# Performance work log

Measured on AMD Instinct MI355X. Metric: run time of the kernel, lower is better.

Reference implementation:

```python
import jax, jax.numpy as jnp
import numpy as np

B, T, S0 = 8, 4, 4096
D_MODEL, H, D, R, RANK = 2048, 16, 128, 64, 512
C = D - R  # content dim = 64


def _rope(x, positions):
    # x: [B, H, T, R]; rotate-half style RoPE as in the torch module
    half = x.shape[-1] // 2
    inv_freq = 1.0 / (10000.0 ** (jnp.arange(half, dtype=jnp.float32) / half))
    freqs = positions.astype(jnp.float32)[:, None] * inv_freq[None, :]  # [T, half]
    cos = jnp.cos(freqs)[None, None].astype(x.dtype)
    sin = jnp.sin(freqs)[None, None].astype(x.dtype)
    x1, x2 = x[..., :half], x[..., half:]
    return jnp.concatenate([x1 * cos - x2 * sin, x1 * sin + x2 * cos], axis=-1)


def setup_inputs() -> dict:
    key = jax.random.key(0)
    ks = jax.random.split(key, 9)
    s = 0.02
    return {
        "x": jax.random.normal(ks[0], (B, T, D_MODEL), jnp.float32),
        "cache_c_kv": jax.random.normal(ks[1], (B, S0, RANK), jnp.float32),
        "cache_k_rope": jax.random.normal(ks[2], (B, S0, H, R), jnp.float32),
        "w_q": jax.random.normal(ks[3], (D_MODEL, H * C), jnp.float32) * s,
        "w_q_rope": jax.random.normal(ks[4], (D_MODEL, H * R), jnp.float32) * s,
        "w_kv_down": jax.random.normal(ks[5], (D_MODEL, RANK), jnp.float32) * s,
        "w_kv_up": jax.random.normal(ks[6], (RANK, H * D), jnp.float32) * s,
        "w_k_rope": jax.random.normal(ks[7], (D_MODEL, H * R), jnp.float32) * s,
        "w_out": jax.random.normal(ks[8], (H * D, D_MODEL), jnp.float32) * s,
    }


def reference(x, cache_c_kv, cache_k_rope, w_q, w_q_rope, w_kv_down, w_kv_up, w_k_rope, w_out):
    cache_len = cache_c_kv.shape[1]
    positions = jnp.arange(cache_len, cache_len + T)

    # queries
    q_content = (x @ w_q).reshape(B, T, H, C).transpose(0, 2, 1, 3)        # [B,H,T,C]
    q_rope = (x @ w_q_rope).reshape(B, T, H, R).transpose(0, 2, 1, 3)      # [B,H,T,R]
    q_rope = _rope(q_rope, positions)
    q = jnp.concatenate([q_content, q_rope], axis=-1)                       # [B,H,T,D]

    # new compressed kv + rope keys, append to cache
    c_kv_new = x @ w_kv_down                                                # [B,T,RANK]
    k_rope_new = (x @ w_k_rope).reshape(B, T, H, R).transpose(0, 2, 1, 3)
    k_rope_new = _rope(k_rope_new, positions).transpose(0, 2, 1, 3)         # [B,T,H,R]
    c_kv = jnp.concatenate([cache_c_kv, c_kv_new], axis=1)                  # [B,S,RANK]
    k_rope = jnp.concatenate([cache_k_rope, k_rope_new], axis=1)            # [B,S,H,R]

    # decompress full cache every step (the expensive MLA pattern)
    S = c_kv.shape[1]
    kv = (c_kv @ w_kv_up).reshape(B, S, H, D)                               # [B,S,H,D]
    k_content = kv[..., :C].transpose(0, 2, 1, 3)                           # [B,H,S,C]
    v = kv.transpose(0, 2, 1, 3)                                            # [B,H,S,D]
    k = jnp.concatenate([k_content, k_rope.transpose(0, 2, 1, 3)], axis=-1) # [B,H,S,D]

    # kv_cache present => is_prefill False => no causal mask (faithful to source)
    scale = 1.0 / jnp.sqrt(jnp.asarray(D, dtype=q.dtype))
    scores = jnp.einsum('bhtd,bhsd->bhts', q, k) * scale
    attn = jax.nn.softmax(scores, axis=-1)
    out = jnp.einsum('bhts,bhsd->bhtd', attn, v)                            # [B,H,T,D]
    out = out.transpose(0, 2, 1, 3).reshape(B, T, H * D)
    return out @ w_out                                                       # [B,T,D_MODEL]
```

## Files before the change

### kernel.cpp

```cpp
#include <hip/hip_runtime.h>
#include <cmath>

#define BB 8
#define TT 4
#define HH 16
#define DDIM 128
#define RRDIM 64
#define CCDIM 64
#define RANKC 512
#define DMODEL 2048
#define S0C 4096
#define NQ 64
#define HD 2048
#define NACT 3584
#define NSC 65
#define SPAD 4160
#define SCALE_ATT 0.08838834764831845f

#define AIDX(row, kk) ((row)*132 + (((row)>>2)<<2) + (kk))

static __device__ __forceinline__ unsigned short f2bf(float x) {
  unsigned u = __float_as_uint(x);
  u += 0x7FFFu + ((u >> 16) & 1u);
  return (unsigned short)(u >> 16);
}
static __device__ __forceinline__ float bf2f(unsigned v16) {
  return __uint_as_float(v16 << 16);
}
static __device__ __forceinline__ unsigned pk2(float a, float b) {
  return (unsigned)f2bf(a) | ((unsigned)f2bf(b) << 16);
}

__global__ __launch_bounds__(256) void k_proj4(const float* __restrict__ A,
                                               const float* __restrict__ w0,
                                               const float* __restrict__ w1,
                                               const float* __restrict__ w2,
                                               const float* __restrict__ w3,
                                               float* __restrict__ part) {
  __shared__ float a_lds[4352];
  const int tid = threadIdx.x;
  const int cb = blockIdx.x;
  const int k0 = blockIdx.y * 128;
  const float* W; int N, lc0, off;
  if (cb < 8)       { W = w0; N = 1024; lc0 = cb * 128;        off = 0; }
  else if (cb < 16) { W = w1; N = 1024; lc0 = (cb - 8) * 128;  off = 1024; }
  else if (cb < 20) { W = w2; N = 512;  lc0 = (cb - 16) * 128; off = 2048; }
  else              { W = w3; N = 1024; lc0 = (cb - 20) * 128; off = 2560; }
  {
    const int row = tid >> 3;
    const int kseg = (tid & 7) * 16;
    const float4* s4 = reinterpret_cast<const float4*>(A + (size_t)row * DMODEL + k0 + kseg);
    float4 v0 = s4[0], v1 = s4[1], v2 = s4[2], v3 = s4[3];
    *reinterpret_cast<float4*>(&a_lds[AIDX(row, kseg)])      = v0;
    *reinterpret_cast<float4*>(&a_lds[AIDX(row, kseg + 4)])  = v1;
    *reinterpret_cast<float4*>(&a_lds[AIDX(row, kseg + 8)])  = v2;
    *reinterpret_cast<float4*>(&a_lds[AIDX(row, kseg + 12)]) = v3;
  }
  __syncthreads();
  const int cg = tid & 31;
  const int rg = tid >> 5;
  float acc[4][4];
  #pragma unroll
  for (int r = 0; r < 4; ++r)
    #pragma unroll
    for (int c = 0; c < 4; ++c) acc[r][c] = 0.f;
  #pragma unroll 4
  for (int kk = 0; kk < 128; ++kk) {
    const float4 w4 = *reinterpret_cast<const float4*>(W + (size_t)(k0 + kk) * N + lc0 + cg * 4);
    const float wv[4] = {w4.x, w4.y, w4.z, w4.w};
    #pragma unroll
    for (int r = 0; r < 4; ++r) {
      const float av = a_lds[AIDX(rg * 4 + r, kk)];
      #pragma unroll
      for (int c = 0; c < 4; ++c) acc[r][c] = fmaf(av, wv[c], acc[r][c]);
    }
  }
  #pragma unroll
  for (int r = 0; r < 4; ++r) {
    float4 o = make_float4(acc[r][0], acc[r][1], acc[r][2], acc[r][3]);
    *reinterpret_cast<float4*>(part + ((size_t)blockIdx.y * 32 + rg * 4 + r) * NACT + off + lc0 + cg * 4) = o;
  }
}

__global__ __launch_bounds__(256) void k_proj(const float* __restrict__ A,
                                              const float* __restrict__ W,
                                              float* __restrict__ part,
                                              int N, int NTOT, int coloff) {
  __shared__ float a_lds[4352];
  const int tid = threadIdx.x;
  const int c0 = blockIdx.x * 128;
  const int k0 = blockIdx.y * 128;
  {
    const int row = tid >> 3;
    const int kseg = (tid & 7) * 16;
    const float4* s4 = reinterpret_cast<const float4*>(A + (size_t)row * DMODEL + k0 + kseg);
    float4 v0 = s4[0], v1 = s4[1], v2 = s4[2], v3 = s4[3];
    *reinterpret_cast<float4*>(&a_lds[AIDX(row, kseg)])      = v0;
    *reinterpret_cast<float4*>(&a_lds[AIDX(row, kseg + 4)])  = v1;
    *reinterpret_cast<float4*>(&a_lds[AIDX(row, kseg + 8)])  = v2;
    *reinterpret_cast<float4*>(&a_lds[AIDX(row, kseg + 12)]) = v3;
  }
  __syncthreads();
  const int cg = tid & 31;
  const int rg = tid >> 5;
  float acc[4][4];
  #pragma unroll
  for (int r = 0; r < 4; ++r)
    #pragma unroll
    for (int c = 0; c < 4; ++c) acc[r][c] = 0.f;
  #pragma unroll 4
  for (int kk = 0; kk < 128; ++kk) {
    const float4 w4 = *reinterpret_cast<const float4*>(W + (size_t)(k0 + kk) * N + c0 + cg * 4);
    const float wv[4] = {w4.x, w4.y, w4.z, w4.w};
    #pragma unroll
    for (int r = 0; r < 4; ++r) {
      const float av = a_lds[AIDX(rg * 4 + r, kk)];
      #pragma unroll
      for (int c = 0; c < 4; ++c) acc[r][c] = fmaf(av, wv[c], acc[r][c]);
    }
  }
  #pragma unroll
  for (int r = 0; r < 4; ++r) {
    float4 o = make_float4(acc[r][0], acc[r][1], acc[r][2], acc[r][3]);
    *reinterpret_cast<float4*>(part + ((size_t)blockIdx.y * 32 + rg * 4 + r) * NTOT + coloff + c0 + cg * 4) = o;
  }
}

__global__ __launch_bounds__(256) void k_reduce(const float* __restrict__ part,
                                                float* __restrict__ out, int total, int nsplit) {
  int g = blockIdx.x * 256 + threadIdx.x;
  if (g >= total) return;
  float s = 0.f;
  #pragma unroll 4
  for (int c = 0; c < nsplit; ++c) s += part[(size_t)c * total + g];
  out[g] = s;
}

__global__ __launch_bounds__(256) void k_qlatrope(const float* __restrict__ act,
                                                  const float* __restrict__ wup,
                                                  float* __restrict__ qlat,
                                                  float* __restrict__ qrope,
                                                  float* __restrict__ ckvn,
                                                  float* __restrict__ krn) {
  __shared__ float wt[64 * 132];
  __shared__ float a_s[32 * 68];
  const int tid = threadIdx.x;
  const int bx = blockIdx.x;
  if (bx < 64) {
    const int h = bx & 15;
    const int r0 = (bx >> 4) * 128;
    {
      const int r = tid >> 1;
      const int cseg = (tid & 1) * 32;
      const float* src = wup + (size_t)(r0 + r) * HD + h * DDIM + cseg;
      #pragma unroll
      for (int u = 0; u < 8; ++u) {
        const float4 v = *reinterpret_cast<const float4*>(src + u * 4);
        wt[(cseg + u * 4 + 0) * 132 + r] = v.x;
        wt[(cseg + u * 4 + 1) * 132 + r] = v.y;
        wt[(cseg + u * 4 + 2) * 132 + r] = v.z;
        wt[(cseg + u * 4 + 3) * 132 + r] = v.w;
      }
    }
    {
      const int bt = tid >> 3;
      const int cseg = (tid & 7) * 8;
      const float4* s4 = reinterpret_cast<const float4*>(act + (size_t)bt * NACT + h * CCDIM + cseg);
      float4 v0 = s4[0], v1 = s4[1];
      *reinterpret_cast<float4*>(&a_s[bt * 68 + cseg])     = v0;
      *reinterpret_cast<float4*>(&a_s[bt * 68 + cseg + 4]) = v1;
    }
    __syncthreads();
    const int r = tid & 127;
    const int bth = tid >> 7;
    float acc[16];
    #pragma unroll
    for (int i = 0; i < 16; ++i) acc[i] = 0.f;
    #pragma unroll 8
    for (int c = 0; c < 64; ++c) {
      const float wv = wt[c * 132 + r];
      #pragma unroll
      for (int i = 0; i < 16; ++i)
        acc[i] = fmaf(a_s[(bth * 16 + i) * 68 + c], wv, acc[i]);
    }
    #pragma unroll
    for (int i = 0; i < 16; ++i) {
      const int bt = bth * 16 + i;
      const int b = bt >> 2, t = bt & 3;
      qlat[((size_t)(b * NQ) + h * TT + t) * RANKC + r0 + r] = acc[i];
    }
    return;
  }
  int g = (bx - 64) * 256 + tid;
  if (g < BB * TT * HH * 32) {
    const int hj = g & 31;
    const int h = (g >> 5) & 15;
    const int t = (g >> 9) & 3;
    const int b = g >> 11;
    const float* arow = act + (size_t)(b * TT + t) * NACT + 1024 + h * RRDIM;
    const float x1 = arow[hj], x2 = arow[hj + 32];
    const double fr = (double)(S0C + t) * pow(10000.0, -(double)hj / 32.0);
    const float cs = (float)cos(fr), sn = (float)sin(fr);
    const int qi = h * TT + t;
    qrope[((size_t)b * NQ + qi) * RRDIM + hj]      = x1 * cs - x2 * sn;
    qrope[((size_t)b * NQ + qi) * RRDIM + hj + 32] = x1 * sn + x2 * cs;
    return;
  }
  g -= BB * TT * HH * 32;
  if (g < BB * TT * HH * 32) {
    const int hj = g & 31;
    const int h = (g >> 5) & 15;
    const int t = (g >> 9) & 3;
    const int b = g >> 11;
    const float* arow = act + (size_t)(b * TT + t) * NACT + 2560 + h * RRDIM;
    const float x1 = arow[hj], x2 = arow[hj + 32];
    const double fr = (double)(S0C + t) * pow(10000.0, -(double)hj / 32.0);
    const float cs = (float)cos(fr), sn = (float)sin(fr);
    krn[((size_t)(b * TT + t) * HH + h) * RRDIM + hj]      = x1 * cs - x2 * sn;
    krn[((size_t)(b * TT + t) * HH + h) * RRDIM + hj + 32] = x1 * sn + x2 * cs;
    return;
  }
  g -= BB * TT * HH * 32;
  if (g < BB * TT * RANKC) {
    ckvn[g] = act[(size_t)(g >> 9) * NACT + 2048 + (g & 511)];
  }
}

__global__ __launch_bounds__(256) void k_rscore(const float* __restrict__ cache_kr,
                                                const float* __restrict__ krn,
                                                const float* __restrict__ qrope,
                                                float* __restrict__ rs) {
  const int bh = blockIdx.x;
  const int b = bh >> 4, h = bh & 15;
  const int tid = threadIdx.x;
  const int ql = tid & 3;
  float4 qf[4][4];
  const float* qrb = qrope + ((size_t)b * NQ + h * TT) * RRDIM;
  #pragma unroll
  for (int t = 0; t < 4; ++t)
    #pragma unroll
    for (int u = 0; u < 4; ++u)
      qf[t][u] = *reinterpret_cast<const float4*>(qrb + t * RRDIM + ql * 16 + u * 4);
  const int s0 = blockIdx.y * 512;
  #pragma unroll 1
  for (int pass = 0; pass < 8; ++pass) {
    const int s = s0 + pass * 64 + (tid >> 2);
    if (s < 4100) {
      const float* krow = (s < S0C)
        ? cache_kr + (((size_t)b * S0C + s) * HH + h) * RRDIM
        : krn + (((size_t)b * TT + (s - S0C)) * HH + h) * RRDIM;
      float p[4] = {0.f, 0.f, 0.f, 0.f};
      #pragma unroll
      for (int u = 0; u < 4; ++u) {
        const float4 kv = *reinterpret_cast<const float4*>(krow + ql * 16 + u * 4);
        #pragma unroll
        for (int t = 0; t < 4; ++t) {
          p[t] += kv.x * qf[t][u].x + kv.y * qf[t][u].y
                + kv.z * qf[t][u].z + kv.w * qf[t][u].w;
        }
      }
      #pragma unroll
      for (int t = 0; t < 4; ++t) {
        p[t] += __shfl_xor(p[t], 1, 4);
        p[t] += __shfl_xor(p[t], 2, 4);
      }
      rs[((size_t)bh * 4 + ql) * SPAD + s] = p[ql];
    }
  }
}

__global__ __launch_bounds__(256) void k_attn(
    const float* __restrict__ cache_ckv, const float* __restrict__ ckvn,
    const float* __restrict__ rs, const float* __restrict__ qlat,
    float* __restrict__ ml, unsigned short* __restrict__ olat) {
  __shared__ float sm[13056];
  float* const A0 = sm;
  float* const A1 = sm + 2176;
  float* const B0 = sm + 4352;
  float* const B1 = sm + 6528;
  float* const p_t = sm + 8704;
  float* const CS0 = sm;
  float* const CS1 = sm + 4352;

  const int tid = threadIdx.x;
  const int ty = tid >> 4, tx = tid & 15;
  const int b = blockIdx.x, chunk = blockIdx.y;
  const int scnt = (chunk < 64) ? 64 : TT;
  const float* ckv = (chunk < 64)
      ? cache_ckv + ((size_t)b * S0C + (size_t)chunk * 64) * RANKC
      : ckvn + (size_t)b * TT * RANKC;
  const float* qlb = qlat + (size_t)b * NQ * RANKC;

  float acc[4][4];
  {
    const int sg = chunk * 64 + tx * 4;
    #pragma unroll
    for (int i = 0; i < 4; ++i) {
      const float4 v = *reinterpret_cast<const float4*>(
          rs + (((size_t)(b * HH + ty)) * 4 + i) * SPAD + sg);
      acc[i][0] = v.x; acc[i][1] = v.y; acc[i][2] = v.z; acc[i][3] = v.w;
    }
  }

  const int row = tid >> 2;
  const int kb = (tid & 3) * 8;
  float4 ra0, ra1, rb0, rb1;
  auto loadAB = [&](int kc) {
    const float4* a4 = reinterpret_cast<const float4*>(qlb + (size_t)row * RANKC + kc + kb);
    ra0 = a4[0]; ra1 = a4[1];
    if (row < scnt) {
      const float4* b4 = reinterpret_cast<const float4*>(ckv + (size_t)row * RANKC + kc + kb);
      rb0 = b4[0]; rb1 = b4[1];
    } else { rb0 = make_float4(0.f, 0.f, 0.f, 0.f); rb1 = rb0; }
  };
  auto writeAB = [&](float* aD, float* bD) {
    aD[(kb+0)*68+row]=ra0.x; aD[(kb+1)*68+row]=ra0.y; aD[(kb+2)*68+row]=ra0.z; aD[(kb+3)*68+row]=ra0.w;
    aD[(kb+4)*68+row]=ra1.x; aD[(kb+5)*68+row]=ra1.y; aD[(kb+6)*68+row]=ra1.z; aD[(kb+7)*68+row]=ra1.w;
    bD[(kb+0)*68+row]=rb0.x; bD[(kb+1)*68+row]=rb0.y; bD[(kb+2)*68+row]=rb0.z; bD[(kb+3)*68+row]=rb0.w;
    bD[(kb+4)*68+row]=rb1.x; bD[(kb+5)*68+row]=rb1.y; bD[(kb+6)*68+row]=rb1.z; bD[(kb+7)*68+row]=rb1.w;
  };
  loadAB(0);
  writeAB(A0, B0);
  __syncthreads();
  for (int kt = 0; kt < 16; ++kt) {
    if (kt < 15) loadAB((kt + 1) * 32);
    const float* aC = (kt & 1) ? A1 : A0;
    const float* bC = (kt & 1) ? B1 : B0;
    #pragma unroll 8
    for (int kk = 0; kk < 32; ++kk) {
      const float4 av = *reinterpret_cast<const float4*>(&aC[kk * 68 + ty * 4]);
      const float4 bv = *reinterpret_cast<const float4*>(&bC[kk * 68 + tx * 4]);
      const float a_[4] = {av.x, av.y, av.z, av.w};
      const float b_[4] = {bv.x, bv.y, bv.z, bv.w};
      #pragma unroll
      for (int i = 0; i < 4; ++i)
        #pragma unroll
        for (int j = 0; j < 4; ++j)
          acc[i][j] = fmaf(a_[i], b_[j], acc[i][j]);
    }
    if (kt < 15) writeAB((kt & 1) ? A0 : A1, (kt & 1) ? B0 : B1);
    __syncthreads();
  }

  #pragma unroll
  for (int i = 0; i < 4; ++i) {
    float mx = -1e30f;
    #pragma unroll
    for (int j = 0; j < 4; ++j) {
      const int s = tx * 4 + j;
      float v = (s < scnt) ? acc[i][j] * SCALE_ATT : -1e30f;
      acc[i][j] = v;
      mx = fmaxf(mx, v);
    }
    #pragma unroll
    for (int off = 1; off < 16; off <<= 1) mx = fmaxf(mx, __shfl_xor(mx, off, 16));
    float sum = 0.f;
    #pragma unroll
    for (int j = 0; j < 4; ++j) {
      const float p = __expf(acc[i][j] - mx);
      acc[i][j] = p;
      sum += p;
    }
    #pragma unroll
    for (int off = 1; off < 16; off <<= 1) sum += __shfl_xor(sum, off, 16);
    #pragma unroll
    for (int j = 0; j < 4; ++j)
      p_t[(tx * 4 + j) * 68 + ty * 4 + i] = acc[i][j];
    if (tx == 0) {
      const size_t mb = (((size_t)b * NSC + chunk) * NQ + ty * 4 + i) * 2;
      ml[mb] = mx; ml[mb + 1] = sum;
    }
  }

  const int sl = tid >> 3;
  const int c16 = (tid & 7) * 16;
  float4 rc0, rc1, rc2, rc3;
  auto loadC = [&](int step) {
    const int rq = step >> 1, sck = step & 1;
    const int s = sck * 32 + sl;
    if (s < scnt) {
      const float4* s4 = reinterpret_cast<const float4*>(ckv + (size_t)s * RANKC + rq * 128 + c16);
      rc0 = s4[0]; rc1 = s4[1]; rc2 = s4[2]; rc3 = s4[3];
    } else { rc0 = make_float4(0.f, 0.f, 0.f, 0.f); rc1 = rc0; rc2 = rc0; rc3 = rc0; }
  };
  auto writeC = [&](float* dst) {
    float4* d4 = reinterpret_cast<float4*>(&dst[sl * 136 + c16]);
    d4[0] = rc0; d4[1] = rc1; d4[2] = rc2; d4[3] = rc3;
  };
  loadC(0);
  writeC(CS0);
  __syncthreads();
  const size_t obase = ((size_t)b * NSC + chunk) * NQ * RANKC;
  float acc2[4][8];
  for (int step = 0; step < 8; ++step) {
    if (step < 7) loadC(step + 1);
    const float* cs = (step & 1) ? CS1 : CS0;
    const int rq = step >> 1, sck = step & 1;
    if (sck == 0) {
      #pragma unroll
      for (int i = 0; i < 4; ++i)
        #pragma unroll
        for (int j = 0; j < 8; ++j) acc2[i][j] = 0.f;
    }
    #pragma unroll 8
    for (int ss = 0; ss < 32; ++ss) {
      const float4 pv = *reinterpret_cast<const float4*>(&p_t[(sck * 32 + ss) * 68 + ty * 4]);
      const float4 c0 = *reinterpret_cast<const float4*>(&cs[ss * 136 + tx * 4]);
      const float4 c1 = *reinterpret_cast<const float4*>(&cs[ss * 136 + 64 + tx * 4]);
      const float p_[4] = {pv.x, pv.y, pv.z, pv.w};
      const float cv[8] = {c0.x, c0.y, c0.z, c0.w, c1.x, c1.y, c1.z, c1.w};
      #pragma unroll
      for (int i = 0; i < 4; ++i)
        #pragma unroll
        for (int j = 0; j < 8; ++j)
          acc2[i][j] = fmaf(p_[i], cv[j], acc2[i][j]);
    }
    if (step < 7) writeC((step & 1) ? CS0 : CS1);
    if (sck == 1) {
      #pragma unroll
      for (int i = 0; i < 4; ++i) {
        const size_t rbase = obase + (size_t)(ty * 4 + i) * RANKC + rq * 128;
        uint2 w0 = make_uint2(pk2(acc2[i][0], acc2[i][1]), pk2(acc2[i][2], acc2[i][3]));
        uint2 w1 = make_uint2(pk2(acc2[i][4], acc2[i][5]), pk2(acc2[i][6], acc2[i][7]));
        *reinterpret_cast<uint2*>(&olat[rbase + tx * 4])      = w0;
        *reinterpret_cast<uint2*>(&olat[rbase + 64 + tx * 4]) = w1;
      }
    }
    __syncthreads();
  }
}

__global__ __launch_bounds__(512) void k_combF(const float* __restrict__ ml,
                                               const unsigned short* __restrict__ olat,
                                               const float* __restrict__ wup,
                                               float* __restrict__ ohead) {
  __shared__ float wrow[4][66];
  __shared__ float att_lds[4][516];
  const int h = blockIdx.x, b = blockIdx.y;
  const int tid = threadIdx.x;
  const int wave = tid >> 6;
  const int i = wave >> 1;
  const int rhalf = wave & 1;
  const int rl = tid & 63;
  const int qi = h * TT + i;
  float m1 = -1e30f, l1 = 0.f, m2 = -1e30f, l2 = 0.f;
  {
    const size_t base = (((size_t)b * NSC + rl) * NQ + qi) * 2;
    m1 = ml[base]; l1 = ml[base + 1];
    if (rl == 0) {
      const size_t b2 = (((size_t)b * NSC + 64) * NQ + qi) * 2;
      m2 = ml[b2]; l2 = ml[b2 + 1];
    }
  }
  float M = fmaxf(m1, m2);
  #pragma unroll
  for (int off = 1; off < 64; off <<= 1) M = fmaxf(M, __shfl_xor(M, off));
  float L = l1 * __expf(m1 - M) + ((rl == 0) ? l2 * __expf(m2 - M) : 0.f);
  #pragma unroll
  for (int off = 1; off < 64; off <<= 1) L += __shfl_xor(L, off);
  const float invL = 1.0f / L;
  wrow[i][rl] = __expf(m1 - M) * invL;
  if (rl == 0) wrow[i][64] = __expf(m2 - M) * invL;
  __syncthreads();
  const int r0 = rhalf * 256 + rl * 4;
  float o0 = 0.f, o1 = 0.f, o2 = 0.f, o3 = 0.f;
  for (int c = 0; c < NSC; ++c) {
    const float w = wrow[i][c];
    const uint2 v = *reinterpret_cast<const uint2*>(
        olat + (((size_t)b * NSC + c) * NQ + qi) * RANKC + r0);
    o0 = fmaf(bf2f(v.x & 0xffffu), w, o0);
    o1 = fmaf(bf2f(v.x >> 16), w, o1);
    o2 = fmaf(bf2f(v.y & 0xffffu), w, o2);
    o3 = fmaf(bf2f(v.y >> 16), w, o3);
  }
  *reinterpret_cast<float4*>(&att_lds[i][r0]) = make_float4(o0, o1, o2, o3);
  __syncthreads();
  const int col = tid & 127;
  const int t = tid >> 7;
  float acc = 0.f;
  #pragma unroll 8
  for (int r = 0; r < RANKC; ++r)
    acc = fmaf(att_lds[t][r], wup[(size_t)r * HD + h * DDIM + col], acc);
  ohead[(size_t)(b * TT + t) * HD + h * DDIM + col] = acc;
}

extern "C" void kernel_launch(void* const* d_in, const int* in_sizes, int n_in,
                              void* d_out, int out_size, void* d_ws, size_t ws_size,
                              hipStream_t stream) {
  const float* x     = (const float*)d_in[0];
  const float* cckv  = (const float*)d_in[1];
  const float* ckr   = (const float*)d_in[2];
  const float* w_q   = (const float*)d_in[3];
  const float* w_qr  = (const float*)d_in[4];
  const float* w_kvd = (const float*)d_in[5];
  const float* w_kvu = (const float*)d_in[6];
  const float* w_kr  = (const float*)d_in[7];
  const float* w_out = (const float*)d_in[8];
  float* out = (float*)d_out;
  float* ws = (float*)d_ws;

  size_t off = 0;
  float* act   = ws + off; off += 32ull * NACT;
  float* qlat  = ws + off; off += (size_t)BB * NQ * RANKC;
  float* qrope = ws + off; off += (size_t)BB * NQ * RRDIM;
  float* ckvn  = ws + off; off += (size_t)BB * TT * RANKC;
  float* krn   = ws + off; off += (size_t)BB * TT * HH * RRDIM;
  float* mlb   = ws + off; off += (size_t)BB * NSC * NQ * 2;
  float* ohead = ws + off; off += 32ull * HD;
  float* rsb   = ws + off; off += 512ull * SPAD;
  float* regB  = ws + off;
  float* part0 = regB;
  unsigned short* olat = (unsigned short*)regB;
  float* part3 = regB;

  k_proj4<<<dim3(28, 16), 256, 0, stream>>>(x, w_q, w_qr, w_kvd, w_kr, part0);
  k_reduce<<<dim3(448), 256, 0, stream>>>(part0, act, 32 * NACT, 16);
  k_qlatrope<<<dim3(256), 256, 0, stream>>>(act, w_kvu, qlat, qrope, ckvn, krn);
  k_rscore<<<dim3(128, 9), 256, 0, stream>>>(ckr, krn, qrope, rsb);

  k_attn<<<dim3(BB, NSC), 256, 0, stream>>>(cckv, ckvn, rsb, qlat, mlb, olat);

  k_combF<<<dim3(16, 8), 512, 0, stream>>>(mlb, olat, w_kvu, ohead);
  k_proj<<<dim3(16, 16), 256, 0, stream>>>(ohead, w_out, part3, 2048, 2048, 0);
  k_reduce<<<dim3(256), 256, 0, stream>>>(part3, out, 32 * HD, 16);
}
```

Before: 221.1 us.

## Use bf16 MFMA in latent attention with pre-transposed bf16 cache

```diff
diff --git a/kernel.cpp b/kernel.cpp
--- a/kernel.cpp
+++ b/kernel.cpp
@@ -1,4 +1,5 @@
 #include <hip/hip_runtime.h>
+#include <hip/hip_fp16.h>
 #include <cmath>
 
 #define BB 8
@@ -16,6 +17,12 @@
 #define NSC 65
 #define SPAD 4160
 #define SCALE_ATT 0.08838834764831845f
+#define LP 72
+#define OLP 136
+
+typedef __attribute__((ext_vector_type(8))) short bf16x8;
+typedef __attribute__((ext_vector_type(4))) float f32x4;
+typedef unsigned short ushortT;
 
 #define AIDX(row, kk) ((row)*132 + (((row)>>2)<<2) + (kk))
 
@@ -31,54 +38,89 @@
   return (unsigned)f2bf(a) | ((unsigned)f2bf(b) << 16);
 }
 
-__global__ __launch_bounds__(256) void k_proj4(const float* __restrict__ A,
+__global__ __launch_bounds__(256) void k_front(const float* __restrict__ A,
                                                const float* __restrict__ w0,
                                                const float* __restrict__ w1,
                                                const float* __restrict__ w2,
                                                const float* __restrict__ w3,
-                                               float* __restrict__ part) {
-  __shared__ float a_lds[4352];
+                                               const float* __restrict__ cckv,
+                                               float* __restrict__ part,
+                                               ushortT* __restrict__ ckvT) {
+  __shared__ float shf[4352];
   const int tid = threadIdx.x;
-  const int cb = blockIdx.x;
-  const int k0 = blockIdx.y * 128;
-  const float* W; int N, lc0, off;
-  if (cb < 8)       { W = w0; N = 1024; lc0 = cb * 128;        off = 0; }
-  else if (cb < 16) { W = w1; N = 1024; lc0 = (cb - 8) * 128;  off = 1024; }
-  else if (cb < 20) { W = w2; N = 512;  lc0 = (cb - 16) * 128; off = 2048; }
-  else              { W = w3; N = 1024; lc0 = (cb - 20) * 128; off = 2560; }
-  {
-    const int row = tid >> 3;
-    const int kseg = (tid & 7) * 16;
-    const float4* s4 = reinterpret_cast<const float4*>(A + (size_t)row * DMODEL + k0 + kseg);
-    float4 v0 = s4[0], v1 = s4[1], v2 = s4[2], v3 = s4[3];
-    *reinterpret_cast<float4*>(&a_lds[AIDX(row, kseg)])      = v0;
-    *reinterpret_cast<float4*>(&a_lds[AIDX(row, kseg + 4)])  = v1;
-    *reinterpret_cast<float4*>(&a_lds[AIDX(row, kseg + 8)])  = v2;
-    *reinterpret_cast<float4*>(&a_lds[AIDX(row, kseg + 12)]) = v3;
-  }
-  __syncthreads();
-  const int cg = tid & 31;
-  const int rg = tid >> 5;
-  float acc[4][4];
-  #pragma unroll
-  for (int r = 0; r < 4; ++r)
-    #pragma unroll
-    for (int c = 0; c < 4; ++c) acc[r][c] = 0.f;
-  #pragma unroll 4
-  for (int kk = 0; kk < 128; ++kk) {
-    const float4 w4 = *reinterpret_cast<const float4*>(W + (size_t)(k0 + kk) * N + lc0 + cg * 4);
-    const float wv[4] = {w4.x, w4.y, w4.z, w4.w};
+  const int bx = blockIdx.x;
+  if (bx < 448) {
+    const int cb = bx % 28;
+    const int k0 = (bx / 28) * 128;
+    const float* W; int N, lc0, off;
+    if (cb < 8)       { W = w0; N = 1024; lc0 = cb * 128;        off = 0; }
+    else if (cb < 16) { W = w1; N = 1024; lc0 = (cb - 8) * 128;  off = 1024; }
+    else if (cb < 20) { W = w2; N = 512;  lc0 = (cb - 16) * 128; off = 2048; }
+    else              { W = w3; N = 1024; lc0 = (cb - 20) * 128; off = 2560; }
+    {
+      const int row = tid >> 3;
+      const int kseg = (tid & 7) * 16;
+      const float4* s4 = reinterpret_cast<const float4*>(A + (size_t)row * DMODEL + k0 + kseg);
+      float4 v0 = s4[0], v1 = s4[1], v2 = s4[2], v3 = s4[3];
+      *reinterpret_cast<float4*>(&shf[AIDX(row, kseg)])      = v0;
+      *reinterpret_cast<float4*>(&shf[AIDX(row, kseg + 4)])  = v1;
+      *reinterpret_cast<float4*>(&shf[AIDX(row, kseg + 8)])  = v2;
+      *reinterpret_cast<float4*>(&shf[AIDX(row, kseg + 12)]) = v3;
+    }
+    __syncthreads();
+    const int cg = tid & 31;
+    const int rg = tid >> 5;
+    float acc[4][4];
+    #pragma unroll
+    for (int r = 0; r < 4; ++r)
+      #pragma unroll
+      for (int c = 0; c < 4; ++c) acc[r][c] = 0.f;
+    #pragma unroll 4
+    for (int kk = 0; kk < 128; ++kk) {
+      const float4 w4 = *reinterpret_cast<const float4*>(W + (size_t)(k0 + kk) * N + lc0 + cg * 4);
+      const float wv[4] = {w4.x, w4.y, w4.z, w4.w};
+      #pragma unroll
+      for (int r = 0; r < 4; ++r) {
+        const float av = shf[AIDX(rg * 4 + r, kk)];
+        #pragma unroll
+        for (int c = 0; c < 4; ++c) acc[r][c] = fmaf(av, wv[c], acc[r][c]);
+      }
+    }
     #pragma unroll
     for (int r = 0; r < 4; ++r) {
-      const float av = a_lds[AIDX(rg * 4 + r, kk)];
-      #pragma unroll
-      for (int c = 0; c < 4; ++c) acc[r][c] = fmaf(av, wv[c], acc[r][c]);
-    }
-  }
-  #pragma unroll
-  for (int r = 0; r < 4; ++r) {
-    float4 o = make_float4(acc[r][0], acc[r][1], acc[r][2], acc[r][3]);
-    *reinterpret_cast<float4*>(part + ((size_t)blockIdx.y * 32 + rg * 4 + r) * NACT + off + lc0 + cg * 4) = o;
+      float4 o = make_float4(acc[r][0], acc[r][1], acc[r][2], acc[r][3]);
+      *reinterpret_cast<float4*>(part + ((size_t)(bx / 28) * 32 + rg * 4 + r) * NACT + off + lc0 + cg * 4) = o;
+    }
+  } else if (bx < 960) {
+    ushortT* tlds = reinterpret_cast<ushortT*>(shf);
+    const int idx = bx - 448;
+    const int b = idx >> 6, c = idx & 63;
+    const float* src = cckv + ((size_t)b * S0C + c * 64) * RANKC;
+    ushortT* dstT = ckvT + ((size_t)(b * NSC + c) * RANKC) * 64;
+    const int s = tid >> 2, rq = tid & 3;
+    const int rloc = tid >> 1, shalf = (tid & 1) * 32;
+    for (int slab = 0; slab < 4; ++slab) {
+      const int r0 = slab * 128;
+      #pragma unroll
+      for (int i = 0; i < 8; ++i) {
+        const float4 v = *reinterpret_cast<const float4*>(src + (size_t)s * RANKC + r0 + rq * 32 + i * 4);
+        *reinterpret_cast<uint2*>(&tlds[s * 136 + rq * 32 + i * 4]) =
+            make_uint2(pk2(v.x, v.y), pk2(v.z, v.w));
+      }
+      __syncthreads();
+      alignas(16) ushortT a[32];
+      #pragma unroll
+      for (int j = 0; j < 32; ++j) a[j] = tlds[(shalf + j) * 136 + rloc];
+      uint4* d = reinterpret_cast<uint4*>(dstT + ((size_t)(r0 + rloc)) * 64 + shalf);
+      const uint4* ap = reinterpret_cast<const uint4*>(a);
+      d[0] = ap[0]; d[1] = ap[1]; d[2] = ap[2]; d[3] = ap[3];
+      __syncthreads();
+    }
+  } else {
+    const int b = bx - 960;
+    uint4* p = reinterpret_cast<uint4*>(ckvT + ((size_t)(b * NSC + 64) * RANKC) * 64);
+    const uint4 z = make_uint4(0, 0, 0, 0);
+    for (int i = tid; i < 2048; i += 256) p[i] = z;
   }
 }
 
@@ -138,10 +180,11 @@
 
 __global__ __launch_bounds__(256) void k_qlatrope(const float* __restrict__ act,
                                                   const float* __restrict__ wup,
-                                                  float* __restrict__ qlat,
+                                                  ushortT* __restrict__ qlat,
                                                   float* __restrict__ qrope,
                                                   float* __restrict__ ckvn,
-                                                  float* __restrict__ krn) {
+                                                  float* __restrict__ krn,
+                                                  ushortT* __restrict__ ckvT) {
   __shared__ float wt[64 * 132];
   __shared__ float a_s[32 * 68];
   const int tid = threadIdx.x;
@@ -187,7 +230,7 @@
     for (int i = 0; i < 16; ++i) {
       const int bt = bth * 16 + i;
       const int b = bt >> 2, t = bt & 3;
-      qlat[((size_t)(b * NQ) + h * TT + t) * RANKC + r0 + r] = acc[i];
+      qlat[((size_t)(b * NQ) + h * TT + t) * RANKC + r0 + r] = f2bf(acc[i]);
     }
     return;
   }
@@ -222,14 +265,19 @@
   }
   g -= BB * TT * HH * 32;
   if (g < BB * TT * RANKC) {
-    ckvn[g] = act[(size_t)(g >> 9) * NACT + 2048 + (g & 511)];
+    const int r = g & 511;
+    const int bt = g >> 9;
+    const int b = bt >> 2, t = bt & 3;
+    const float v = act[(size_t)bt * NACT + 2048 + r];
+    ckvn[g] = v;
+    ckvT[(((size_t)(b * NSC + 64) * RANKC) + r) * 64 + t] = f2bf(v);
   }
 }
 
 __global__ __launch_bounds__(256) void k_rscore(const float* __restrict__ cache_kr,
                                                 const float* __restrict__ krn,
                                                 const float* __restrict__ qrope,
-                                                float* __restrict__ rs) {
+                                                __half* __restrict__ rs) {
   const int bh = blockIdx.x;
   const int b = bh >> 4, h = bh & 15;
   const int tid = threadIdx.x;
@@ -264,174 +312,188 @@
         p[t] += __shfl_xor(p[t], 1, 4);
         p[t] += __shfl_xor(p[t], 2, 4);
       }
-      rs[((size_t)bh * 4 + ql) * SPAD + s] = p[ql];
+      rs[((size_t)bh * 4 + ql) * SPAD + s] = __float2half(p[ql] * SCALE_ATT);
     }
   }
 }
 
 __global__ __launch_bounds__(256) void k_attn(
     const float* __restrict__ cache_ckv, const float* __restrict__ ckvn,
-    const float* __restrict__ rs, const float* __restrict__ qlat,
-    float* __restrict__ ml, unsigned short* __restrict__ olat) {
-  __shared__ float sm[13056];
-  float* const A0 = sm;
-  float* const A1 = sm + 2176;
-  float* const B0 = sm + 4352;
-  float* const B1 = sm + 6528;
-  float* const p_t = sm + 8704;
-  float* const CS0 = sm;
-  float* const CS1 = sm + 4352;
+    const ushortT* __restrict__ qlat, const ushortT* __restrict__ ckvT,
+    const __half* __restrict__ rs, float* __restrict__ ml,
+    ushortT* __restrict__ olat) {
+  __shared__ ushortT smem[23040];
+  ushortT* const QA0 = smem;
+  ushortT* const QA1 = smem + 4608;
+  ushortT* const KB0 = smem + 9216;
+  ushortT* const KB1 = smem + 13824;
+  ushortT* const CT  = smem;
+  ushortT* const OL  = smem + 9216;
+  ushortT* const PL  = smem + 18432;
 
   const int tid = threadIdx.x;
-  const int ty = tid >> 4, tx = tid & 15;
+  const int lane = tid & 63;
+  const int wv = tid >> 6;
+  const int m0 = wv * 16;
+  const int lm = lane & 15;
+  const int lg = lane >> 4;
   const int b = blockIdx.x, chunk = blockIdx.y;
   const int scnt = (chunk < 64) ? 64 : TT;
-  const float* ckv = (chunk < 64)
+  const float* bsrc = (chunk < 64)
       ? cache_ckv + ((size_t)b * S0C + (size_t)chunk * 64) * RANKC
       : ckvn + (size_t)b * TT * RANKC;
-  const float* qlb = qlat + (size_t)b * NQ * RANKC;
-
-  float acc[4][4];
-  {
-    const int sg = chunk * 64 + tx * 4;
-    #pragma unroll
-    for (int i = 0; i < 4; ++i) {
-      const float4 v = *reinterpret_cast<const float4*>(
-          rs + (((size_t)(b * HH + ty)) * 4 + i) * SPAD + sg);
-      acc[i][0] = v.x; acc[i][1] = v.y; acc[i][2] = v.z; acc[i][3] = v.w;
-    }
-  }
-
-  const int row = tid >> 2;
-  const int kb = (tid & 3) * 8;
-  float4 ra0, ra1, rb0, rb1;
-  auto loadAB = [&](int kc) {
-    const float4* a4 = reinterpret_cast<const float4*>(qlb + (size_t)row * RANKC + kc + kb);
-    ra0 = a4[0]; ra1 = a4[1];
-    if (row < scnt) {
-      const float4* b4 = reinterpret_cast<const float4*>(ckv + (size_t)row * RANKC + kc + kb);
-      rb0 = b4[0]; rb1 = b4[1];
-    } else { rb0 = make_float4(0.f, 0.f, 0.f, 0.f); rb1 = rb0; }
+  const ushortT* qsrc = qlat + (size_t)b * NQ * RANKC;
+
+  float rv[4][4];
+  #pragma unroll
+  for (int reg = 0; reg < 4; ++reg) {
+    const int q = m0 + lg * 4 + reg;
+    const __half* rp = rs + ((size_t)(b * HH + (q >> 2)) * TT + (q & 3)) * SPAD + chunk * 64;
+    #pragma unroll
+    for (int st = 0; st < 4; ++st)
+      rv[reg][st] = __half2float(rp[st * 16 + lm]);
+  }
+
+  const int srow = tid >> 2;
+  const int rseg = (tid & 3) * 16;
+  uint4 qreg[2];
+  float4 kreg[4];
+  auto loadStageA = [&](int kt) {
+    const uint4* qp = reinterpret_cast<const uint4*>(qsrc + (size_t)srow * RANKC + kt * 64 + rseg);
+    qreg[0] = qp[0]; qreg[1] = qp[1];
+    if (srow < scnt) {
+      const float4* kp = reinterpret_cast<const float4*>(bsrc + (size_t)srow * RANKC + kt * 64 + rseg);
+      kreg[0] = kp[0]; kreg[1] = kp[1]; kreg[2] = kp[2]; kreg[3] = kp[3];
+    } else {
+      kreg[0] = make_float4(0.f, 0.f, 0.f, 0.f); kreg[1] = kreg[0]; kreg[2] = kreg[0]; kreg[3] = kreg[0];
+    }
   };
-  auto writeAB = [&](float* aD, float* bD) {
-    aD[(kb+0)*68+row]=ra0.x; aD[(kb+1)*68+row]=ra0.y; aD[(kb+2)*68+row]=ra0.z; aD[(kb+3)*68+row]=ra0.w;
-    aD[(kb+4)*68+row]=ra1.x; aD[(kb+5)*68+row]=ra1.y; aD[(kb+6)*68+row]=ra1.z; aD[(kb+7)*68+row]=ra1.w;
-    bD[(kb+0)*68+row]=rb0.x; bD[(kb+1)*68+row]=rb0.y; bD[(kb+2)*68+row]=rb0.z; bD[(kb+3)*68+row]=rb0.w;
-    bD[(kb+4)*68+row]=rb1.x; bD[(kb+5)*68+row]=rb1.y; bD[(kb+6)*68+row]=rb1.z; bD[(kb+7)*68+row]=rb1.w;
+  auto writeStageA = [&](ushortT* qa, ushortT* kb) {
+    *reinterpret_cast<uint4*>(&qa[srow * LP + rseg])     = qreg[0];
+    *reinterpret_cast<uint4*>(&qa[srow * LP + rseg + 8]) = qreg[1];
+    *reinterpret_cast<uint4*>(&kb[srow * LP + rseg]) =
+        make_uint4(pk2(kreg[0].x, kreg[0].y), pk2(kreg[0].z, kreg[0].w),
+                   pk2(kreg[1].x, kreg[1].y), pk2(kreg[1].z, kreg[1].w));
+    *reinterpret_cast<uint4*>(&kb[srow * LP + rseg + 8]) =
+        make_uint4(pk2(kreg[2].x, kreg[2].y), pk2(kreg[2].z, kreg[2].w),
+                   pk2(kreg[3].x, kreg[3].y), pk2(kreg[3].z, kreg[3].w));
   };
-  loadAB(0);
-  writeAB(A0, B0);
+
+  f32x4 acc[4];
+  #pragma unroll
+  for (int st = 0; st < 4; ++st) acc[st] = (f32x4){0.f, 0.f, 0.f, 0.f};
+
+  loadStageA(0);
+  writeStageA(QA0, KB0);
+  loadStageA(1);
   __syncthreads();
-  for (int kt = 0; kt < 16; ++kt) {
-    if (kt < 15) loadAB((kt + 1) * 32);
-    const float* aC = (kt & 1) ? A1 : A0;
-    const float* bC = (kt & 1) ? B1 : B0;
-    #pragma unroll 8
-    for (int kk = 0; kk < 32; ++kk) {
-      const float4 av = *reinterpret_cast<const float4*>(&aC[kk * 68 + ty * 4]);
-      const float4 bv = *reinterpret_cast<const float4*>(&bC[kk * 68 + tx * 4]);
-      const float a_[4] = {av.x, av.y, av.z, av.w};
-      const float b_[4] = {bv.x, bv.y, bv.z, bv.w};
-      #pragma unroll
-      for (int i = 0; i < 4; ++i)
-        #pragma unroll
-        for (int j = 0; j < 4; ++j)
-          acc[i][j] = fmaf(a_[i], b_[j], acc[i][j]);
-    }
-    if (kt < 15) writeAB((kt & 1) ? A0 : A1, (kt & 1) ? B0 : B1);
+  for (int kt = 0; kt < 8; ++kt) {
+    if (kt < 7) {
+      writeStageA((kt & 1) ? QA0 : QA1, (kt & 1) ? KB0 : KB1);
+      if (kt < 6) loadStageA(kt + 2);
+    }
+    const ushortT* qa = (kt & 1) ? QA1 : QA0;
+    const ushortT* kb = (kt & 1) ? KB1 : KB0;
+    #pragma unroll
+    for (int ks = 0; ks < 2; ++ks) {
+      const bf16x8 af = *reinterpret_cast<const bf16x8*>(&qa[(m0 + lm) * LP + ks * 32 + lg * 8]);
+      #pragma unroll
+      for (int st = 0; st < 4; ++st) {
+        const bf16x8 bfv = *reinterpret_cast<const bf16x8*>(&kb[(st * 16 + lm) * LP + ks * 32 + lg * 8]);
+        acc[st] = __builtin_amdgcn_mfma_f32_16x16x32_bf16(af, bfv, acc[st], 0, 0, 0);
+      }
+    }
     __syncthreads();
   }
 
-  #pragma unroll
-  for (int i = 0; i < 4; ++i) {
+  const ushortT* ctsrc = ckvT + ((size_t)(b * NSC + chunk) * RANKC) * 64;
+  const int rloc = tid >> 1;
+  const int shalf = (tid & 1) * 32;
+  uint4 creg[4];
+  auto loadCT = [&](int rg) {
+    const uint4* p = reinterpret_cast<const uint4*>(ctsrc + ((size_t)(rg * 128 + rloc)) * 64 + shalf);
+    creg[0] = p[0]; creg[1] = p[1]; creg[2] = p[2]; creg[3] = p[3];
+  };
+  auto writeCT = [&]() {
+    uint4* d = reinterpret_cast<uint4*>(&CT[rloc * LP + shalf]);
+    d[0] = creg[0]; d[1] = creg[1]; d[2] = creg[2]; d[3] = creg[3];
+  };
+  loadCT(0);
+
+  #pragma unroll
+  for (int reg = 0; reg < 4; ++reg) {
+    const int q = m0 + lg * 4 + reg;
+    float vv[4];
     float mx = -1e30f;
     #pragma unroll
-    for (int j = 0; j < 4; ++j) {
-      const int s = tx * 4 + j;
-      float v = (s < scnt) ? acc[i][j] * SCALE_ATT : -1e30f;
-      acc[i][j] = v;
-      mx = fmaxf(mx, v);
+    for (int st = 0; st < 4; ++st) {
+      const int sl = st * 16 + lm;
+      const float val = (sl < scnt) ? fmaf(acc[st][reg], SCALE_ATT, rv[reg][st]) : -1e30f;
+      vv[st] = val;
+      mx = fmaxf(mx, val);
     }
     #pragma unroll
     for (int off = 1; off < 16; off <<= 1) mx = fmaxf(mx, __shfl_xor(mx, off, 16));
     float sum = 0.f;
     #pragma unroll
-    for (int j = 0; j < 4; ++j) {
-      const float p = __expf(acc[i][j] - mx);
-      acc[i][j] = p;
+    for (int st = 0; st < 4; ++st) {
+      const float p = __expf(vv[st] - mx);
+      vv[st] = p;
       sum += p;
     }
     #pragma unroll
     for (int off = 1; off < 16; off <<= 1) sum += __shfl_xor(sum, off, 16);
     #pragma unroll
-    for (int j = 0; j < 4; ++j)
-      p_t[(tx * 4 + j) * 68 + ty * 4 + i] = acc[i][j];
-    if (tx == 0) {
-      const size_t mb = (((size_t)b * NSC + chunk) * NQ + ty * 4 + i) * 2;
+    for (int st = 0; st < 4; ++st)
+      PL[q * LP + st * 16 + lm] = f2bf(vv[st]);
+    if (lm == 0) {
+      const size_t mb = (((size_t)b * NSC + chunk) * NQ + q) * 2;
       ml[mb] = mx; ml[mb + 1] = sum;
     }
   }
-
-  const int sl = tid >> 3;
-  const int c16 = (tid & 7) * 16;
-  float4 rc0, rc1, rc2, rc3;
-  auto loadC = [&](int step) {
-    const int rq = step >> 1, sck = step & 1;
-    const int s = sck * 32 + sl;
-    if (s < scnt) {
-      const float4* s4 = reinterpret_cast<const float4*>(ckv + (size_t)s * RANKC + rq * 128 + c16);
-      rc0 = s4[0]; rc1 = s4[1]; rc2 = s4[2]; rc3 = s4[3];
-    } else { rc0 = make_float4(0.f, 0.f, 0.f, 0.f); rc1 = rc0; rc2 = rc0; rc3 = rc0; }
-  };
-  auto writeC = [&](float* dst) {
-    float4* d4 = reinterpret_cast<float4*>(&dst[sl * 136 + c16]);
-    d4[0] = rc0; d4[1] = rc1; d4[2] = rc2; d4[3] = rc3;
-  };
-  loadC(0);
-  writeC(CS0);
   __syncthreads();
-  const size_t obase = ((size_t)b * NSC + chunk) * NQ * RANKC;
-  float acc2[4][8];
-  for (int step = 0; step < 8; ++step) {
-    if (step < 7) loadC(step + 1);
-    const float* cs = (step & 1) ? CS1 : CS0;
-    const int rq = step >> 1, sck = step & 1;
-    if (sck == 0) {
-      #pragma unroll
-      for (int i = 0; i < 4; ++i)
-        #pragma unroll
-        for (int j = 0; j < 8; ++j) acc2[i][j] = 0.f;
-    }
-    #pragma unroll 8
-    for (int ss = 0; ss < 32; ++ss) {
-      const float4 pv = *reinterpret_cast<const float4*>(&p_t[(sck * 32 + ss) * 68 + ty * 4]);
-      const float4 c0 = *reinterpret_cast<const float4*>(&cs[ss * 136 + tx * 4]);
-      const float4 c1 = *reinterpret_cast<const float4*>(&cs[ss * 136 + 64 + tx * 4]);
-      const float p_[4] = {pv.x, pv.y, pv.z, pv.w};
-      const float cv[8] = {c0.x, c0.y, c0.z, c0.w, c1.x, c1.y, c1.z, c1.w};
-      #pragma unroll
-      for (int i = 0; i < 4; ++i)
-        #pragma unroll
-        for (int j = 0; j < 8; ++j)
-          acc2[i][j] = fmaf(p_[i], cv[j], acc2[i][j]);
-    }
-    if (step < 7) writeC((step & 1) ? CS0 : CS1);
-    if (sck == 1) {
-      #pragma unroll
-      for (int i = 0; i < 4; ++i) {
-        const size_t rbase = obase + (size_t)(ty * 4 + i) * RANKC + rq * 128;
-        uint2 w0 = make_uint2(pk2(acc2[i][0], acc2[i][1]), pk2(acc2[i][2], acc2[i][3]));
-        uint2 w1 = make_uint2(pk2(acc2[i][4], acc2[i][5]), pk2(acc2[i][6], acc2[i][7]));
-        *reinterpret_cast<uint2*>(&olat[rbase + tx * 4])      = w0;
-        *reinterpret_cast<uint2*>(&olat[rbase + 64 + tx * 4]) = w1;
-      }
-    }
+
+  writeCT();
+  loadCT(1);
+  const bf16x8 pa0 = *reinterpret_cast<const bf16x8*>(&PL[(m0 + lm) * LP + lg * 8]);
+  const bf16x8 pa1 = *reinterpret_cast<const bf16x8*>(&PL[(m0 + lm) * LP + 32 + lg * 8]);
+  __syncthreads();
+
+  const size_t obase = ((size_t)(b * NSC + chunk) * NQ) * RANKC;
+  for (int rg = 0; rg < 4; ++rg) {
+    f32x4 a2[8];
+    #pragma unroll
+    for (int nt = 0; nt < 8; ++nt) a2[nt] = (f32x4){0.f, 0.f, 0.f, 0.f};
+    #pragma unroll
+    for (int nt = 0; nt < 8; ++nt) {
+      const bf16x8 b0 = *reinterpret_cast<const bf16x8*>(&CT[(nt * 16 + lm) * LP + lg * 8]);
+      const bf16x8 b1 = *reinterpret_cast<const bf16x8*>(&CT[(nt * 16 + lm) * LP + 32 + lg * 8]);
+      a2[nt] = __builtin_amdgcn_mfma_f32_16x16x32_bf16(pa0, b0, a2[nt], 0, 0, 0);
+      a2[nt] = __builtin_amdgcn_mfma_f32_16x16x32_bf16(pa1, b1, a2[nt], 0, 0, 0);
+    }
+    #pragma unroll
+    for (int nt = 0; nt < 8; ++nt)
+      #pragma unroll
+      for (int reg = 0; reg < 4; ++reg)
+        OL[(m0 + lg * 4 + reg) * OLP + nt * 16 + lm] = f2bf(a2[nt][reg]);
     __syncthreads();
+    {
+      const int q = tid >> 2;
+      const int seg = (tid & 3) * 32;
+      const uint4* s4 = reinterpret_cast<const uint4*>(&OL[q * OLP + seg]);
+      uint4* d4 = reinterpret_cast<uint4*>(&olat[obase + (size_t)q * RANKC + rg * 128 + seg]);
+      d4[0] = s4[0]; d4[1] = s4[1]; d4[2] = s4[2]; d4[3] = s4[3];
+    }
+    if (rg < 3) {
+      writeCT();
+      if (rg < 2) loadCT(rg + 2);
+      __syncthreads();
+    }
   }
 }
 
 __global__ __launch_bounds__(512) void k_combF(const float* __restrict__ ml,
-                                               const unsigned short* __restrict__ olat,
+                                               const ushortT* __restrict__ olat,
                                                const float* __restrict__ wup,
                                                float* __restrict__ ohead) {
   __shared__ float wrow[4][66];
@@ -500,25 +562,26 @@
   float* ws = (float*)d_ws;
 
   size_t off = 0;
-  float* act   = ws + off; off += 32ull * NACT;
-  float* qlat  = ws + off; off += (size_t)BB * NQ * RANKC;
-  float* qrope = ws + off; off += (size_t)BB * NQ * RRDIM;
-  float* ckvn  = ws + off; off += (size_t)BB * TT * RANKC;
-  float* krn   = ws + off; off += (size_t)BB * TT * HH * RRDIM;
-  float* mlb   = ws + off; off += (size_t)BB * NSC * NQ * 2;
-  float* ohead = ws + off; off += 32ull * HD;
-  float* rsb   = ws + off; off += 512ull * SPAD;
+  float* act      = ws + off; off += 32ull * NACT;
+  ushortT* qlat   = (ushortT*)(ws + off); off += 131072;
+  float* qrope    = ws + off; off += 32768;
+  float* ckvn     = ws + off; off += 16384;
+  float* krn      = ws + off; off += 32768;
+  float* mlb      = ws + off; off += (size_t)BB * NSC * NQ * 2;
+  float* ohead    = ws + off; off += 65536;
+  __half* rsb     = (__half*)(ws + off); off += 1064960;
+  ushortT* ckvT   = (ushortT*)(ws + off); off += 8519680;
   float* regB  = ws + off;
   float* part0 = regB;
-  unsigned short* olat = (unsigned short*)regB;
+  ushortT* olat = (ushortT*)regB;
   float* part3 = regB;
 
-  k_proj4<<<dim3(28, 16), 256, 0, stream>>>(x, w_q, w_qr, w_kvd, w_kr, part0);
+  k_front<<<dim3(968), 256, 0, stream>>>(x, w_q, w_qr, w_kvd, w_kr, cckv, part0, ckvT);
   k_reduce<<<dim3(448), 256, 0, stream>>>(part0, act, 32 * NACT, 16);
-  k_qlatrope<<<dim3(256), 256, 0, stream>>>(act, w_kvu, qlat, qrope, ckvn, krn);
+  k_qlatrope<<<dim3(256), 256, 0, stream>>>(act, w_kvu, qlat, qrope, ckvn, krn, ckvT);
   k_rscore<<<dim3(128, 9), 256, 0, stream>>>(ckr, krn, qrope, rsb);
 
-  k_attn<<<dim3(BB, NSC), 256, 0, stream>>>(cckv, ckvn, rsb, qlat, mlb, olat);
+  k_attn<<<dim3(BB, NSC), 256, 0, stream>>>(cckv, ckvn, qlat, ckvT, rsb, mlb, olat);
 
   k_combF<<<dim3(16, 8), 512, 0, stream>>>(mlb, olat, w_kvu, ohead);
   k_proj<<<dim3(16, 16), 256, 0, stream>>>(ohead, w_out, part3, 2048, 2048, 0);
```

Result: slower. 241.6 us (+9.3%).
